# Performance work log

Measured on AMD Instinct MI355X. Metric: run time of the kernel, lower is better.

## Reference

```python
import jax, jax.numpy as jnp
import numpy as np

SIZE = 32  # CDIM internal attention resolution
DN = ('NCHW', 'OIHW', 'NCHW')


def conv3(x, w):
    # 3x3 (or matching SAME-size) conv, stride 1, padding SAME, no bias
    return jax.lax.conv_general_dilated(x, w, (1, 1), 'SAME', dimension_numbers=DN)


def bconv(x, w, s, b):
    # BBasicConv2d with BatchNorm folded (eval mode) into per-channel scale s and bias b, then ReLU
    return jax.nn.relu(conv3(x, w) * s[None, :, None, None] + b[None, :, None, None])


def spa_att(x, w):
    # SpatialAttention: sigmoid(conv([mean_c, max_c])) * x + x
    avg = jnp.mean(x, axis=1, keepdims=True)
    mx = jnp.max(x, axis=1, keepdims=True)
    a = conv3(jnp.concatenate([avg, mx], axis=1), w)
    return jax.nn.sigmoid(a) * x + x


def resize_bicubic(x, h, w):
    return jax.image.resize(x, (x.shape[0], x.shape[1], h, w), method='cubic')


def setup_inputs() -> dict:
    key = jax.random.key(0)
    ks = iter(jax.random.split(key, 64))
    B, C, H, W = 16, 64, 128, 128
    d = {}
    d['x'] = jax.random.normal(next(ks), (B, C, H, W), jnp.float32)
    d['y'] = jax.random.normal(next(ks), (B, C, H, W), jnp.float32)
    def qkv_params(pfx, cin):
        d[pfx + '_w'] = jax.random.normal(next(ks), (C, cin, 3, 3), jnp.float32) * 0.05
        d[pfx + '_s'] = jax.random.uniform(next(ks), (C,), jnp.float32, 0.5, 1.5)
        d[pfx + '_b'] = jax.random.normal(next(ks), (C,), jnp.float32) * 0.05
    for pfx in ['rq', 'rk', 'rv', 'iq', 'ik', 'iv']:
        qkv_params(pfx, C)
    d['red_w'] = jax.random.normal(next(ks), (C, 4 * C, 3, 3), jnp.float32) * 0.03
    d['red_s'] = jax.random.uniform(next(ks), (C,), jnp.float32, 0.5, 1.5)
    d['red_b'] = jax.random.normal(next(ks), (C,), jnp.float32) * 0.05
    d['sec_w'] = jax.random.normal(next(ks), (C, 3 * C, 3, 3), jnp.float32) * 0.03
    d['sec_s'] = jax.random.uniform(next(ks), (C,), jnp.float32, 0.5, 1.5)
    d['sec_b'] = jax.random.normal(next(ks), (C,), jnp.float32) * 0.05
    for g in ['g1', 'g2', 'g3', 'g4']:
        d[g] = jax.random.normal(next(ks), (1,), jnp.float32) * 0.1
    d['sa_r_w'] = jax.random.normal(next(ks), (1, 2, 3, 3), jnp.float32) * 0.1
    d['sa_i_w'] = jax.random.normal(next(ks), (1, 2, 3, 3), jnp.float32) * 0.1
    return d


def reference(x, y,
              rq_w, rq_s, rq_b, rk_w, rk_s, rk_b, rv_w, rv_s, rv_b,
              iq_w, iq_s, iq_b, ik_w, ik_s, ik_b, iv_w, iv_s, iv_b,
              red_w, red_s, red_b, sec_w, sec_s, sec_b,
              g1, g2, g3, g4, sa_r_w, sa_i_w):
    B, C, H, W = x.shape
    S = SIZE
    x_re = resize_bicubic(x, S, S)
    y_re = resize_bicubic(y, S, S)

    def qkv(z, qw, qs, qb, kw, ks_, kb, vw, vs, vb):
        Q = bconv(z, qw, qs, qb).reshape(B, -1, S * S)   # [B,C,S2]
        K = bconv(z, kw, ks_, kb).reshape(B, -1, S * S)  # [B,C,S2] (torch permutes later)
        V = bconv(z, vw, vs, vb).reshape(B, -1, S * S)
        return Q, K, V

    RQ, RK, RV = qkv(x_re, rq_w, rq_s, rq_b, rk_w, rk_s, rk_b, rv_w, rv_s, rv_b)
    IQ, IK, IV = qkv(y_re, iq_w, iq_s, iq_b, ik_w, ik_s, ik_b, iv_w, iv_s, iv_b)
    DV = RV + IV

    def attn(Q, K, V, orig, g):
        # mask = softmax(K^T @ Q, axis=-1): [B,S2,S2]
        mask = jax.nn.softmax(jnp.einsum('bcs,bct->bst', K, Q), axis=-1)
        # refine = V @ mask^T -> [B,C,S2]
        refine = jnp.einsum('bct,bst->bcs', V, mask).reshape(B, -1, S, S)
        refine = g.reshape(()) * refine
        return resize_bicubic(refine, orig.shape[2], orig.shape[3]) + orig

    RGB_refine = attn(RQ, RK, DV, x, g1)
    INF_refine = attn(IQ, IK, DV, y, g2)
    RGB_INF_refine = attn(RQ, IK, RV, y, g3)
    INF_RGB_refine = attn(IQ, RK, IV, x, g4)

    GLOBAL_ATT = bconv(jnp.concatenate([RGB_refine, INF_refine, RGB_INF_refine, INF_RGB_refine], axis=1),
                       red_w, red_s, red_b)
    rgb_spa = spa_att(x, sa_r_w)
    inf_spa = spa_att(y, sa_i_w)
    out = bconv(jnp.concatenate([GLOBAL_ATT, inf_spa, rgb_spa], axis=1), sec_w, sec_s, sec_b)
    return out
```

## Files before the change

kernel.cpp:

```cpp
#include <hip/hip_runtime.h>
#include <hip/hip_bf16.h>

#define B 16
#define C 64
#define H 128
#define W 128
#define S 32
#define S2 1024
#define HW 16384

typedef __attribute__((ext_vector_type(8))) short bf16x8;
typedef __attribute__((ext_vector_type(4))) float f32x4;
typedef __attribute__((ext_vector_type(8))) unsigned short u16x8;
typedef __attribute__((ext_vector_type(4))) unsigned short u16x4;

static __device__ __forceinline__ unsigned short f2bf(float v) {
    __hip_bfloat16 h = __float2bfloat16(v);
    return *reinterpret_cast<unsigned short*>(&h);
}
static __device__ __forceinline__ float bf2f(unsigned short u) {
    union { unsigned int i; float f; } cv;
    cv.i = ((unsigned int)u) << 16;
    return cv.f;
}

__device__ __forceinline__ float keys(float t) {
    t = fabsf(t);
    if (t >= 2.f) return 0.f;
    float t2 = t * t, t3 = t2 * t;
    if (t >= 1.f) return -0.5f * t3 + 2.5f * t2 - 4.f * t + 2.f;
    return 1.5f * t3 - 2.5f * t2 + 1.f;
}

__global__ void k_init(float* __restrict__ wd, float* __restrict__ wu) {
    int tid = threadIdx.x;
    if (tid < 32) {
        int i = tid;
        float sf = 4.f * i + 1.5f;
        int j0 = 4 * i - 6;
        float w[16];
        float s = 0.f;
        for (int k = 0; k < 16; k++) {
            int j = j0 + k;
            float v = 0.f;
            if (j >= 0 && j < 128) v = keys((sf - (float)j) * 0.25f);
            w[k] = v; s += v;
        }
        float inv = 1.f / s;
        for (int k = 0; k < 16; k++) wd[i * 16 + k] = w[k] * inv;
    } else if (tid >= 64 && tid < 192) {
        int i = tid - 64;
        float sf = 0.25f * i - 0.375f;
        int j0 = (int)floorf(sf) - 1;
        float w[4];
        float s = 0.f;
        for (int k = 0; k < 4; k++) {
            int j = j0 + k;
            float v = 0.f;
            if (j >= 0 && j < 32) v = keys(sf - (float)j);
            w[k] = v; s += v;
        }
        float inv = 1.f / s;
        for (int k = 0; k < 4; k++) wu[i * 4 + k] = w[k] * inv;
    }
}

__global__ void __launch_bounds__(256) k_down(const float* __restrict__ x, const float* __restrict__ y,
                                              const float* __restrict__ wd, unsigned short* __restrict__ re) {
    int bid = blockIdx.x;
    int img = bid >> 10;
    int bc = bid & 1023;
    const float* src = (img ? y : x) + (size_t)bc * HW;
    __shared__ unsigned short xsrc[128 * 128];
    __shared__ float tmp[32 * 160];
    __shared__ float wsh[512];
    int tid = threadIdx.x;
    for (int i = tid; i < 512; i += 256) wsh[i] = wd[i];
    #pragma unroll
    for (int it = 0; it < 16; ++it) {
        int i4 = (tid + it * 256) * 4;
        float4 v = *reinterpret_cast<const float4*>(src + i4);
        u16x4 o = {f2bf(v.x), f2bf(v.y), f2bf(v.z), f2bf(v.w)};
        *reinterpret_cast<u16x4*>(&xsrc[i4]) = o;
    }
    __syncthreads();
    #pragma unroll
    for (int it = 0; it < 16; ++it) {
        int idx = tid + it * 256;
        int oy = idx >> 7, xx = idx & 127;
        int j0 = 4 * oy - 6;
        float acc = 0.f;
        #pragma unroll
        for (int k = 0; k < 16; k++) {
            int j = j0 + k;
            if (j >= 0 && j < 128) acc += wsh[oy * 16 + k] * bf2f(xsrc[j * 128 + xx]);
        }
        tmp[oy * 160 + (xx & 3) * 40 + (xx >> 2)] = acc;
    }
    __syncthreads();
    #pragma unroll
    for (int it = 0; it < 4; ++it) {
        int idx = tid + it * 256;
        int oy = idx >> 5, ox = idx & 31;
        int j0 = 4 * ox - 6;
        float acc = 0.f;
        #pragma unroll
        for (int k = 0; k < 16; k++) {
            int j = j0 + k;
            if (j >= 0 && j < 128) acc += wsh[ox * 16 + k] * tmp[oy * 160 + (j & 3) * 40 + (j >> 2)];
        }
        re[(size_t)bid * 1024 + idx] = f2bf(acc);
    }
}

__global__ void k_wpack(const float* __restrict__ w, const float* __restrict__ s,
                        unsigned short* __restrict__ wpk, int cin) {
    int ks = blockIdx.x;
    int tid = threadIdx.x;
    int lane = tid & 63, ct = tid >> 6;
    int cb = ks / 9, kk = ks % 9;
    int m = ct * 16 + (lane & 15);
    int qq = lane >> 4;
    float sc = s[m];
    u16x8 outv;
    #pragma unroll
    for (int j = 0; j < 8; ++j) {
        int k = qq * 4 + (j & 3) + ((j >> 2) << 4);
        int ci = cb * 32 + k;
        float v = w[((size_t)m * cin + ci) * 9 + kk] * sc;
        outv[j] = f2bf(v);
    }
    *reinterpret_cast<u16x8*>(wpk + ((size_t)(ks * 4 + ct) * 64 + lane) * 8) = outv;
}

__global__ void k_wpackc(const float* __restrict__ w, const float* __restrict__ s,
                         unsigned short* __restrict__ wpk, int cin) {
    int ks = blockIdx.x;
    int tid = threadIdx.x;
    int lane = tid & 63, ct = tid >> 6;
    int cb = ks / 9, kk = ks % 9;
    int m = ct * 16 + (lane & 15);
    int qq = (lane >> 4) & 3;
    float sc = s[m];
    u16x8 outv;
    #pragma unroll
    for (int j = 0; j < 8; ++j) {
        int ci = cb * 32 + qq * 8 + j;
        float v = w[((size_t)m * cin + ci) * 9 + kk] * sc;
        outv[j] = f2bf(v);
    }
    *reinterpret_cast<u16x8*>(wpk + ((size_t)(ks * 4 + ct) * 64 + lane) * 8) = outv;
}

struct QkvBias { const float* b[6]; };

__global__ void __launch_bounds__(256) k_qkv2(const unsigned short* __restrict__ re,
                                              const unsigned short* __restrict__ wpkq,
                                              QkvBias bias,
                                              unsigned short* __restrict__ qt,
                                              unsigned short* __restrict__ kt,
                                              unsigned short* __restrict__ vn) {
    int bid = blockIdx.x;
    int q = bid >> 6;
    int rem = bid & 63;
    int b = rem >> 2;
    int quad = rem & 3;
    int img = (q < 3) ? 0 : 1;
    const unsigned short* src = re + ((size_t)(img * 16 + b)) * 64 * 1024;
    const bf16x8* wp = reinterpret_cast<const bf16x8*>(wpkq + (size_t)q * 18 * 4 * 64 * 8);
    const float* bptr = bias.b[q];

    int tid = threadIdx.x;
    int lane = tid & 63, w = tid >> 6;
    int l15 = lane & 15, qg = lane >> 4;

    __shared__ __align__(16) unsigned short xs[10 * 34 * 32];

    if (tid < 160) {
        int r = tid >> 4;
        int inner = tid & 15;
        int col = (inner >> 3) ? 33 : 0;
        int qd = inner & 7;
        int sbase = ((qd & 3) << 3) + ((qd >> 2) << 2);
        int sbs = sbase ^ ((((col >> 1) & 3)) << 3);
        u16x4 z = {0, 0, 0, 0};
        *reinterpret_cast<u16x4*>(&xs[(r * 34 + col) * 32 + sbs]) = z;
    }

    f32x4 acc[4][4] = {};

    for (int cb = 0; cb < 2; ++cb) {
        __syncthreads();
        #pragma unroll
        for (int tt = 0; tt < 2; ++tt) {
            int task = tid + tt * 256;
            if (task < 320) {
                int r = task >> 5;
                int inner = task & 31;
                int qd = inner >> 2, xc = inner & 3;
                int yy = quad * 8 - 1 + r;
                int x0 = xc * 8;
                int ci0 = cb * 32 + qd * 4;
                u16x8 v0, v1, v2, v3;
                if (yy >= 0 && yy < 32) {
                    const unsigned short* sp = src + (size_t)ci0 * 1024 + yy * 32 + x0;
                    v0 = *reinterpret_cast<const u16x8*>(sp);
                    v1 = *reinterpret_cast<const u16x8*>(sp + 1024);
                    v2 = *reinterpret_cast<const u16x8*>(sp + 2048);
                    v3 = *reinterpret_cast<const u16x8*>(sp + 3072);
                } else {
                    v0 = (u16x8)0; v1 = (u16x8)0; v2 = (u16x8)0; v3 = (u16x8)0;
                }
                int sbase = ((qd & 3) << 3) + ((qd >> 2) << 2);
                #pragma unroll
                for (int dx = 0; dx < 8; ++dx) {
                    int col = x0 + 1 + dx;
                    int sbs = sbase ^ (((col >> 1) & 3) << 3);
                    u16x4 pk = {v0[dx], v1[dx], v2[dx], v3[dx]};
                    *reinterpret_cast<u16x4*>(&xs[(r * 34 + col) * 32 + sbs]) = pk;
                }
            }
        }
        __syncthreads();
        #pragma unroll
        for (int ky = 0; ky < 3; ++ky) {
            #pragma unroll
            for (int kx = 0; kx < 3; ++kx) {
                int ksidx = cb * 9 + ky * 3 + kx;
                bf16x8 afr[4];
                #pragma unroll
                for (int ct = 0; ct < 4; ++ct)
                    afr[ct] = wp[((size_t)(ksidx * 4 + ct) << 6) + lane];
                bf16x8 bfr[4];
                #pragma unroll
                for (int nt = 0; nt < 4; ++nt) {
                    int rp = nt >> 1;
                    int col = (nt & 1) * 16 + l15 + kx;
                    int r = w * 2 + rp + ky;
                    int sbs = (qg ^ ((col >> 1) & 3)) << 3;
                    bfr[nt] = *reinterpret_cast<const bf16x8*>(&xs[(r * 34 + col) * 32 + sbs]);
                }
                #pragma unroll
                for (int ct = 0; ct < 4; ++ct)
                    #pragma unroll
                    for (int nt = 0; nt < 4; ++nt)
                        acc[ct][nt] = __builtin_amdgcn_mfma_f32_16x16x32_bf16(afr[ct], bfr[nt], acc[ct][nt], 0, 0, 0);
            }
        }
    }

    int pair = (q < 3) ? 0 : 1;
    bool isV = (q == 2 || q == 5);
    unsigned short* dst;
    if (q == 0 || q == 3)      dst = qt + ((size_t)(pair * 16 + b)) * 65536;
    else if (q == 1 || q == 4) dst = kt + ((size_t)(pair * 16 + b)) * 65536;
    else                       dst = vn + ((size_t)(pair * 16 + b)) * 65536;
    #pragma unroll
    for (int ct = 0; ct < 4; ++ct) {
        float4 bi = *reinterpret_cast<const float4*>(bptr + ct * 16 + qg * 4);
        #pragma unroll
        for (int nt = 0; nt < 4; ++nt) {
            int pxl = nt * 16 + l15;
            int rowg = quad * 8 + w * 2 + (pxl >> 5);
            int colg = pxl & 31;
            int px = rowg * 32 + colg;
            #pragma unroll
            for (int reg = 0; reg < 4; ++reg) {
                int co = ct * 16 + qg * 4 + reg;
                float bv = (reg == 0) ? bi.x : (reg == 1) ? bi.y : (reg == 2) ? bi.z : bi.w;
                float v = fmaxf(acc[ct][nt][reg] + bv, 0.f);
                unsigned short bf = f2bf(v);
                if (isV) dst[(size_t)co * 1024 + px] = bf;
                else     dst[(size_t)px * 64 + co] = bf;
            }
        }
    }
}

__global__ void k_packa(const unsigned short* __restrict__ qt,
                        const unsigned short* __restrict__ kt,
                        unsigned short* __restrict__ qtf,
                        unsigned short* __restrict__ ktf) {
    int bid = blockIdx.x;
    int tsel = bid >> 7;
    int b = (bid >> 3) & 15;
    int seg = bid & 7;
    int tid = threadIdx.x;
    int lane = tid & 63, w = tid >> 6;
    int l15 = lane & 15, qg = lane >> 4;
    const unsigned short* src = (tsel < 2 ? qt : kt) + ((size_t)((tsel & 1) * 16 + b)) * 65536;
    unsigned short* dst = (tsel < 2 ? qtf : ktf) + ((size_t)((tsel & 1) * 16 + b)) * 65536;
    #pragma unroll
    for (int it = 0; it < 4; ++it) {
        int fi = seg * 16 + it * 4 + w;
        int tf = fi >> 1, kb = fi & 1;
        const unsigned short* row = src + (size_t)(tf * 16 + l15) * 64 + kb * 32 + qg * 4;
        u16x4 a0 = *reinterpret_cast<const u16x4*>(row);
        u16x4 a1 = *reinterpret_cast<const u16x4*>(row + 16);
        u16x8 o;
        #pragma unroll
        for (int j = 0; j < 4; ++j) { o[j] = a0[j]; o[4 + j] = a1[j]; }
        *reinterpret_cast<u16x8*>(dst + (size_t)fi * 512 + lane * 8) = o;
    }
}

__global__ void k_packv(const unsigned short* __restrict__ vn,
                        unsigned short* __restrict__ vf) {
    int bid = blockIdx.x;
    int b = bid >> 3;
    int seg = bid & 7;
    int tid = threadIdx.x;
    int lane = tid & 63, w = tid >> 6;
    int l15 = lane & 15, qg = lane >> 4;
    const unsigned short* rv = vn + (size_t)b * 65536;
    const unsigned short* iv = vn + (size_t)(16 + b) * 65536;
    #pragma unroll
    for (int it = 0; it < 4; ++it) {
        int fi = seg * 16 + it * 4 + w;
        int cf = fi >> 5, tq = fi & 31;
        int c = cf * 16 + l15;
        size_t roff = (size_t)c * 1024 + tq * 32 + qg * 4;
        u16x4 r0 = *reinterpret_cast<const u16x4*>(rv + roff);
        u16x4 r1 = *reinterpret_cast<const u16x4*>(rv + roff + 16);
        u16x4 i0 = *reinterpret_cast<const u16x4*>(iv + roff);
        u16x4 i1 = *reinterpret_cast<const u16x4*>(iv + roff + 16);
        u16x8 orv, oiv, odv;
        #pragma unroll
        for (int j = 0; j < 4; ++j) {
            orv[j] = r0[j]; orv[4 + j] = r1[j];
            oiv[j] = i0[j]; oiv[4 + j] = i1[j];
            odv[j] = f2bf(bf2f(r0[j]) + bf2f(i0[j]));
            odv[4 + j] = f2bf(bf2f(r1[j]) + bf2f(i1[j]));
        }
        size_t eoff = ((size_t)b * 128 + fi) * 512 + lane * 8;
        *reinterpret_cast<u16x8*>(vf + eoff) = orv;
        *reinterpret_cast<u16x8*>(vf + 1048576 + eoff) = oiv;
        *reinterpret_cast<u16x8*>(vf + 2097152 + eoff) = odv;
    }
}

__global__ void __launch_bounds__(256) k_attn3(const unsigned short* __restrict__ QTF,
                                               const unsigned short* __restrict__ KTF,
                                               const unsigned short* __restrict__ VF,
                                               float* __restrict__ ref) {
    int bid = blockIdx.x;
    int a = bid >> 10;
    int b = (bid >> 6) & 15;
    int stile = bid & 63;
    int qsel = (a == 0 || a == 2) ? 0 : 1;
    int ksel = (a == 0 || a == 3) ? 0 : 1;
    int vsel = (a < 2) ? 2 : (a == 2 ? 0 : 1);

    int tid = threadIdx.x;
    int lane = tid & 63, w = tid >> 6;
    int l15 = lane & 15, qg = lane >> 4;

    const bf16x8* qf = reinterpret_cast<const bf16x8*>(QTF) + ((size_t)(qsel * 16 + b) * 128) * 64;
    const bf16x8* kf = reinterpret_cast<const bf16x8*>(KTF) + ((size_t)(ksel * 16 + b) * 128) * 64;
    const bf16x8* vfb = reinterpret_cast<const bf16x8*>(VF) + ((size_t)(vsel * 16 + b) * 128) * 64;

    __shared__ float mxw[4][16];
    __shared__ float smw[4][16];
    __shared__ float rbuf[4][64 * 16];

    bf16x8 bk0 = kf[(size_t)(stile * 2 + 0) * 64 + lane];
    bf16x8 bk1 = kf[(size_t)(stile * 2 + 1) * 64 + lane];
    f32x4 acc[16] = {};
    #pragma unroll
    for (int mf = 0; mf < 16; ++mf) {
        int tf = w * 16 + mf;
        bf16x8 a0 = qf[(size_t)(tf * 2 + 0) * 64 + lane];
        bf16x8 a1 = qf[(size_t)(tf * 2 + 1) * 64 + lane];
        acc[mf] = __builtin_amdgcn_mfma_f32_16x16x32_bf16(a0, bk0, acc[mf], 0, 0, 0);
        acc[mf] = __builtin_amdgcn_mfma_f32_16x16x32_bf16(a1, bk1, acc[mf], 0, 0, 0);
    }

    float mx = -1e30f;
    #pragma unroll
    for (int mf = 0; mf < 16; ++mf)
        #pragma unroll
        for (int r = 0; r < 4; ++r) mx = fmaxf(mx, acc[mf][r]);
    mx = fmaxf(mx, __shfl_xor(mx, 16));
    mx = fmaxf(mx, __shfl_xor(mx, 32));
    if (qg == 0) mxw[w][l15] = mx;
    __syncthreads();
    float M = fmaxf(fmaxf(mxw[0][l15], mxw[1][l15]), fmaxf(mxw[2][l15], mxw[3][l15]));
    float sm = 0.f;
    #pragma unroll
    for (int mf = 0; mf < 16; ++mf)
        #pragma unroll
        for (int r = 0; r < 4; ++r) {
            float e = __builtin_amdgcn_exp2f((acc[mf][r] - M) * 1.4426950408889634f);
            acc[mf][r] = e;
            sm += e;
        }
    sm += __shfl_xor(sm, 16);
    sm += __shfl_xor(sm, 32);
    if (qg == 0) smw[w][l15] = sm;
    __syncthreads();
    float inv = 1.f / (smw[0][l15] + smw[1][l15] + smw[2][l15] + smw[3][l15]);

    f32x4 pacc[4] = {};
    #pragma unroll
    for (int kk = 0; kk < 8; ++kk) {
        bf16x8 bp;
        #pragma unroll
        for (int j = 0; j < 4; ++j) {
            bp[j] = (short)f2bf(acc[2 * kk][j]);
            bp[4 + j] = (short)f2bf(acc[2 * kk + 1][j]);
        }
        #pragma unroll
        for (int cf = 0; cf < 4; ++cf) {
            bf16x8 av = vfb[(size_t)(cf * 32 + w * 8 + kk) * 64 + lane];
            pacc[cf] = __builtin_amdgcn_mfma_f32_16x16x32_bf16(av, bp, pacc[cf], 0, 0, 0);
        }
    }
    #pragma unroll
    for (int cf = 0; cf < 4; ++cf)
        #pragma unroll
        for (int r = 0; r < 4; ++r)
            rbuf[w][(cf * 16 + qg * 4 + r) * 16 + l15] = pacc[cf][r] * inv;
    __syncthreads();

    {
        int c = tid >> 2, sg = tid & 3;
        f32x4 o;
        #pragma unroll
        for (int k2 = 0; k2 < 4; ++k2) {
            int idx = c * 16 + sg * 4 + k2;
            o[k2] = rbuf[0][idx] + rbuf[1][idx] + rbuf[2][idx] + rbuf[3][idx];
        }
        *reinterpret_cast<f32x4*>(ref + (((size_t)a * 16 + b) * 64 + c) * 1024 + stile * 16 + sg * 4) = o;
    }
}

__global__ void __launch_bounds__(256) k_up3(const float* __restrict__ ref, const float* __restrict__ wu,
                                             const float* __restrict__ x, const float* __restrict__ y,
                                             const float* __restrict__ g1, const float* __restrict__ g2,
                                             const float* __restrict__ g3, const float* __restrict__ g4,
                                             __hip_bfloat16* __restrict__ cat4) {
    int bid = blockIdx.x;
    int b = bid >> 7;
    int c = (bid >> 1) & 63;
    int pair = bid & 1;
    int aA = pair ? 1 : 0;
    int aB = pair ? 2 : 3;
    const float* orig = (pair ? y : x) + ((size_t)b * 64 + c) * HW;
    float gA = (pair ? g2 : g1)[0];
    float gB = (pair ? g3 : g4)[0];
    const float* srcA = ref + (((size_t)aA * 16 + b) * 64 + c) * 1024;
    const float* srcB = ref + (((size_t)aB * 16 + b) * 64 + c) * 1024;

    __shared__ float wsh[512];
    __shared__ float rch[2][1024];
    __shared__ float tmp[2][128][32];
    int tid = threadIdx.x;
    for (int i = tid; i < 512; i += 256) wsh[i] = wu[i];
    {
        float4 a4 = reinterpret_cast<const float4*>(srcA)[tid];
        float4 b4 = reinterpret_cast<const float4*>(srcB)[tid];
        reinterpret_cast<float4*>(&rch[0][0])[tid] = a4;
        reinterpret_cast<float4*>(&rch[1][0])[tid] = b4;
    }
    __syncthreads();

    #pragma unroll
    for (int it = 0; it < 4; ++it) {
        int task = tid + it * 256;
        int u = task >> 5, xx = task & 31;
        float w0[5], w1[5];
        #pragma unroll
        for (int m = 0; m < 5; ++m) {
            int j = u - 2 + m;
            bool ok = (j >= 0) && (j < 32);
            w0[m] = ok ? rch[0][j * 32 + xx] : 0.f;
            w1[m] = ok ? rch[1][j * 32 + xx] : 0.f;
        }
        #pragma unroll
        for (int r = 0; r < 4; ++r) {
            int oy = 4 * u + r;
            int mo = r >> 1;
            float a0 = 0.f, a1 = 0.f;
            #pragma unroll
            for (int k = 0; k < 4; ++k) {
                float wv = wsh[oy * 4 + k];
                a0 += wv * w0[mo + k];
                a1 += wv * w1[mo + k];
            }
            tmp[0][oy][xx] = a0;
            tmp[1][oy][xx] = a1;
        }
    }
    __syncthreads();

    size_t obA = ((size_t)b * 256 + aA * 64 + c) * HW;
    size_t obB = ((size_t)b * 256 + aB * 64 + c) * HW;
    unsigned short* cat = (unsigned short*)cat4;
    #pragma unroll
    for (int it = 0; it < 16; ++it) {
        int task = tid + it * 256;
        int oy = task >> 5, t = task & 31;
        float u0[5], u1[5];
        #pragma unroll
        for (int m = 0; m < 5; ++m) {
            int j = t - 2 + m;
            bool ok = (j >= 0) && (j < 32);
            u0[m] = ok ? tmp[0][oy][j] : 0.f;
            u1[m] = ok ? tmp[1][oy][j] : 0.f;
        }
        float4 ov = *reinterpret_cast<const float4*>(orig + oy * 128 + t * 4);
        float ovr[4] = {ov.x, ov.y, ov.z, ov.w};
        u16x4 oA, oB;
        #pragma unroll
        for (int r = 0; r < 4; ++r) {
            int ox = 4 * t + r;
            int mo = r >> 1;
            float a0 = 0.f, a1 = 0.f;
            #pragma unroll
            for (int k = 0; k < 4; ++k) {
                float wv = wsh[ox * 4 + k];
                a0 += wv * u0[mo + k];
                a1 += wv * u1[mo + k];
            }
            oA[r] = f2bf(gA * a0 + ovr[r]);
            oB[r] = f2bf(gB * a1 + ovr[r]);
        }
        *reinterpret_cast<u16x4*>(&cat[obA + oy * 128 + t * 4]) = oA;
        *reinterpret_cast<u16x4*>(&cat[obB + oy * 128 + t * 4]) = oB;
    }
}

__global__ void k_mm(const float* __restrict__ x, const float* __restrict__ y,
                     float* __restrict__ mm) {
    int bid = blockIdx.x;
    int img = bid >> 7;
    int rem = bid & 127;
    int b = rem >> 3;
    int chunk = rem & 7;
    const float* src = (img ? y : x) + (size_t)b * 64 * HW;
    int tid = threadIdx.x;
    size_t base = ((size_t)(img * 16 + b)) * 2 * HW;
    for (int i = 0; i < 8; i++) {
        int px = chunk * 2048 + i * 256 + tid;
        float s = 0.f, mx = -1e30f;
        for (int c = 0; c < 64; c++) {
            float v = src[(size_t)c * HW + px];
            s += v;
            mx = fmaxf(mx, v);
        }
        mm[base + px] = s * (1.f / 64.f);
        mm[base + HW + px] = mx;
    }
}

__global__ void k_spaconv(const float* __restrict__ mm, const float* __restrict__ saw_r,
                          const float* __restrict__ saw_i, float* __restrict__ sig) {
    int bid = blockIdx.x;
    int img = bid >> 7;
    int rem = bid & 127;
    int b = rem >> 3;
    int chunk = rem & 7;
    const float* w = img ? saw_i : saw_r;
    __shared__ float wsh[18];
    if (threadIdx.x < 18) wsh[threadIdx.x] = w[threadIdx.x];
    __syncthreads();
    const float* m0 = mm + ((size_t)(img * 16 + b)) * 2 * HW;
    for (int i = 0; i < 8; i++) {
        int px = chunk * 2048 + i * 256 + threadIdx.x;
        int yy = px >> 7, xx = px & 127;
        float acc = 0.f;
        #pragma unroll
        for (int ch = 0; ch < 2; ch++) {
            const float* m = m0 + (size_t)ch * HW;
            #pragma unroll
            for (int dy = 0; dy < 3; dy++)
                #pragma unroll
                for (int dx = 0; dx < 3; dx++) {
                    int iy = yy + dy - 1, ix = xx + dx - 1;
                    if (iy >= 0 && iy < 128 && ix >= 0 && ix < 128)
                        acc += wsh[ch * 9 + dy * 3 + dx] * m[iy * 128 + ix];
                }
        }
        sig[((size_t)(img * 16 + b)) * HW + px] = 1.f / (1.f + expf(-acc));
    }
}

__global__ void k_scale(const float* __restrict__ x, const float* __restrict__ y,
                        const float* __restrict__ sig, unsigned short* __restrict__ sxy) {
    int gid = blockIdx.x * 256 + threadIdx.x;
    int part = gid >> 21;
    int b = (gid >> 17) & 15;
    int c = (gid >> 11) & 63;
    int t8 = gid & 2047;
    int px = t8 * 8;
    const float* src = (part ? x : y) + ((size_t)b * 64 + c) * HW + px;
    const float* sg = sig + ((size_t)((part ? 0 : 16) + b)) * HW + px;
    u16x8 o;
    #pragma unroll
    for (int j = 0; j < 8; ++j) o[j] = f2bf(src[j] * (1.f + sg[j]));
    *reinterpret_cast<u16x8*>(sxy + ((size_t)b * 128 + part * 64 + c) * HW + px) = o;
}

template<int CIBLKS, bool OBF16>
__global__ void __launch_bounds__(512, 1) k_conv(const unsigned short* __restrict__ srcA, int cinA,
                                                 const unsigned short* __restrict__ srcB,
                                                 const unsigned short* __restrict__ wpk,
                                                 const float* __restrict__ bias,
                                                 void* __restrict__ outp) {
    const int cinB = CIBLKS * 32 - cinA;
    int bid = blockIdx.x;
    int b = bid >> 5, rt = bid & 31;
    int y0 = rt * 4;
    int tid = threadIdx.x;
    int lane = tid & 63, w = tid >> 6;
    int l15 = lane & 15, qg = (lane >> 4) & 3;
    int wr = w >> 1, wc = w & 1;

    __shared__ __align__(16) unsigned short xs[6 * 133 * 32];
    __shared__ __align__(16) unsigned short ws2[9 * 4 * 64 * 8];

    if (tid < 48) {
        int r = tid >> 3;
        int rem = tid & 7;
        int col = (rem >> 2) ? 129 : 0;
        int q = rem & 3;
        int slot = q ^ ((col >> 2) & 3);
        u16x8 z = (u16x8)0;
        *reinterpret_cast<u16x8*>(&xs[(r * 133 + col) * 32 + slot * 8]) = z;
    }

    f32x4 acc[4][4] = {};
    const bf16x8* wp = reinterpret_cast<const bf16x8*>(wpk);

    for (int cb = 0; cb < CIBLKS; ++cb) {
        __syncthreads();
        {
            const bf16x8* wsrc = wp + (size_t)cb * 2304;
            bf16x8* wdst = reinterpret_cast<bf16x8*>(ws2);
            #pragma unroll
            for (int e = 0; e < 4; ++e)
                wdst[tid + e * 512] = wsrc[tid + e * 512];
            if (tid < 256) wdst[tid + 2048] = wsrc[tid + 2048];
        }
        #pragma unroll
        for (int tt = 0; tt < 2; ++tt) {
            int task = tid + tt * 512;
            if (task < 768) {
                int q8 = task / 192;
                int rr = (task % 192) >> 5;
                int xq = task & 31;
                int yy = y0 - 1 + rr;
                int x0 = xq * 4;
                int ci0 = cb * 32 + q8 * 8;
                u16x4 v[8];
                if (yy >= 0 && yy < 128) {
                    const unsigned short* sp;
                    if (ci0 < cinA) sp = srcA + ((size_t)b * cinA + ci0) * HW;
                    else            sp = srcB + ((size_t)b * cinB + (ci0 - cinA)) * HW;
                    sp += yy * 128 + x0;
                    #pragma unroll
                    for (int p = 0; p < 8; ++p)
                        v[p] = *reinterpret_cast<const u16x4*>(sp + p * HW);
                } else {
                    #pragma unroll
                    for (int p = 0; p < 8; ++p) v[p] = (u16x4)0;
                }
                #pragma unroll
                for (int i = 0; i < 4; ++i) {
                    int d = (i + xq) & 3;
                    int col = x0 + 1 + d;
                    int slot = q8 ^ ((col >> 2) & 3);
                    u16x8 o;
                    #pragma unroll
                    for (int p = 0; p < 8; ++p) o[p] = v[p][d];
                    *reinterpret_cast<u16x8*>(&xs[(rr * 133 + col) * 32 + slot * 8]) = o;
                }
            }
        }
        __syncthreads();
        __builtin_amdgcn_s_setprio(1);
        #pragma unroll
        for (int ky = 0; ky < 3; ++ky) {
            #pragma unroll
            for (int kx = 0; kx < 3; ++kx) {
                int kk = ky * 3 + kx;
                bf16x8 afr[4];
                #pragma unroll
                for (int ct = 0; ct < 4; ++ct)
                    afr[ct] = *reinterpret_cast<const bf16x8*>(&ws2[((kk * 4 + ct) * 64 + lane) * 8]);
                int row = wr + ky;
                bf16x8 bfr[4];
                #pragma unroll
                for (int nt = 0; nt < 4; ++nt) {
                    int col = wc * 64 + nt * 16 + l15 + kx;
                    int slot = qg ^ ((col >> 2) & 3);
                    bfr[nt] = *reinterpret_cast<const bf16x8*>(&xs[(row * 133 + col) * 32 + slot * 8]);
                }
                #pragma unroll
                for (int ct = 0; ct < 4; ++ct)
                    #pragma unroll
                    for (int nt = 0; nt < 4; ++nt)
                        acc[ct][nt] = __builtin_amdgcn_mfma_f32_16x16x32_bf16(afr[ct], bfr[nt], acc[ct][nt], 0, 0, 0);
            }
        }
        __builtin_amdgcn_s_setprio(0);
    }

    int row_out = y0 + wr;
    #pragma unroll
    for (int ct = 0; ct < 4; ++ct) {
        float4 bi = *reinterpret_cast<const float4*>(bias + ct * 16 + qg * 4);
        #pragma unroll
        for (int nt = 0; nt < 4; ++nt) {
            int col_out = wc * 64 + nt * 16 + l15;
            #pragma unroll
            for (int reg = 0; reg < 4; ++reg) {
                int co = ct * 16 + qg * 4 + reg;
                float bv = (reg == 0) ? bi.x : (reg == 1) ? bi.y : (reg == 2) ? bi.z : bi.w;
                float v = fmaxf(acc[ct][nt][reg] + bv, 0.f);
                size_t off = ((size_t)b * 64 + co) * HW + row_out * 128 + col_out;
                if (OBF16) ((unsigned short*)outp)[off] = f2bf(v);
                else       ((float*)outp)[off] = v;
            }
        }
    }
}

extern "C" void kernel_launch(void* const* d_in, const int* in_sizes, int n_in,
                              void* d_out, int out_size, void* d_ws, size_t ws_size,
                              hipStream_t stream) {
    const float* x = (const float*)d_in[0];
    const float* y = (const float*)d_in[1];

    const float* qw[6]; const float* qs[6];
    QkvBias qb;
    for (int q = 0; q < 6; q++) {
        qw[q] = (const float*)d_in[2 + 3 * q];
        qs[q] = (const float*)d_in[3 + 3 * q];
        qb.b[q] = (const float*)d_in[4 + 3 * q];
    }
    const float* red_w = (const float*)d_in[20];
    const float* red_s = (const float*)d_in[21];
    const float* red_b = (const float*)d_in[22];
    const float* sec_w = (const float*)d_in[23];
    const float* sec_s = (const float*)d_in[24];
    const float* sec_b = (const float*)d_in[25];
    const float* g1 = (const float*)d_in[26];
    const float* g2 = (const float*)d_in[27];
    const float* g3 = (const float*)d_in[28];
    const float* g4 = (const float*)d_in[29];
    const float* sa_r_w = (const float*)d_in[30];
    const float* sa_i_w = (const float*)d_in[31];

    float* WD = (float*)d_ws;
    float* WU = WD + 512;
    float* SIG = WU + 512;
    float* MM = SIG + 524288;
    float* REF = MM + 1048576;
    unsigned short* WPKR = (unsigned short*)(REF + 4194304);
    unsigned short* WPKS = WPKR + 147456;
    unsigned short* WPKQ = WPKS + 110592;
    unsigned short* REB = WPKQ + 221184;
    unsigned short* QT  = REB + 2097152;
    unsigned short* KT  = QT + 2097152;
    unsigned short* VN  = KT + 2097152;
    unsigned short* GATT = VN + 2097152;
    unsigned short* CAT4 = GATT + 16777216;
    unsigned short* QTF = CAT4;
    unsigned short* KTF = CAT4 + 2097152;
    unsigned short* VF  = CAT4 + 4194304;
    unsigned short* SECXY = CAT4;

    k_init<<<1, 256, 0, stream>>>(WD, WU);
    k_down<<<2 * 16 * 64, 256, 0, stream>>>(x, y, WD, REB);
    for (int q = 0; q < 6; q++)
        k_wpack<<<18, 256, 0, stream>>>(qw[q], qs[q], WPKQ + (size_t)q * 36864, 64);
    k_wpackc<<<72, 256, 0, stream>>>(red_w, red_s, WPKR, 256);
    k_wpackc<<<54, 256, 0, stream>>>(sec_w, sec_s, WPKS, 192);
    k_qkv2<<<6 * 64, 256, 0, stream>>>(REB, WPKQ, qb, QT, KT, VN);
    k_packa<<<512, 256, 0, stream>>>(QT, KT, QTF, KTF);
    k_packv<<<128, 256, 0, stream>>>(VN, VF);
    k_attn3<<<4 * 16 * 64, 256, 0, stream>>>(QTF, KTF, VF, REF);
    k_up3<<<16 * 128, 256, 0, stream>>>(REF, WU, x, y, g1, g2, g3, g4, (__hip_bfloat16*)CAT4);
    k_mm<<<2 * 16 * 8, 256, 0, stream>>>(x, y, MM);
    k_spaconv<<<2 * 16 * 8, 256, 0, stream>>>(MM, sa_r_w, sa_i_w, SIG);
    k_conv<8, true><<<16 * 32, 512, 0, stream>>>(CAT4, 256, CAT4, WPKR, red_b, GATT);
    k_scale<<<16384, 256, 0, stream>>>(x, y, SIG, SECXY);
    k_conv<6, false><<<16 * 32, 512, 0, stream>>>(GATT, 64, SECXY, WPKS, sec_b, d_out);
}
```

Before: 556.3 us.

## Halve conv weight LDS buffer to fit two blocks per CU, change swizzle

```diff
diff --git a/kernel.cpp b/kernel.cpp
--- a/kernel.cpp
+++ b/kernel.cpp
@@ -602,7 +602,7 @@
 }
 
 template<int CIBLKS, bool OBF16>
-__global__ void __launch_bounds__(512, 1) k_conv(const unsigned short* __restrict__ srcA, int cinA,
+__global__ void __launch_bounds__(512, 2) k_conv(const unsigned short* __restrict__ srcA, int cinA,
                                                  const unsigned short* __restrict__ srcB,
                                                  const unsigned short* __restrict__ wpk,
                                                  const float* __restrict__ bias,
@@ -617,30 +617,29 @@
     int wr = w >> 1, wc = w & 1;
 
     __shared__ __align__(16) unsigned short xs[6 * 133 * 32];
-    __shared__ __align__(16) unsigned short ws2[9 * 4 * 64 * 8];
+    __shared__ __align__(16) unsigned short ws2[5 * 4 * 64 * 8];
 
     if (tid < 48) {
         int r = tid >> 3;
         int rem = tid & 7;
         int col = (rem >> 2) ? 129 : 0;
         int q = rem & 3;
-        int slot = q ^ ((col >> 2) & 3);
+        int slot = q ^ (((col >> 2) ^ (col >> 4)) & 3);
         u16x8 z = (u16x8)0;
         *reinterpret_cast<u16x8*>(&xs[(r * 133 + col) * 32 + slot * 8]) = z;
     }
 
     f32x4 acc[4][4] = {};
     const bf16x8* wp = reinterpret_cast<const bf16x8*>(wpk);
+    bf16x8* wdst = reinterpret_cast<bf16x8*>(ws2);
 
     for (int cb = 0; cb < CIBLKS; ++cb) {
         __syncthreads();
         {
             const bf16x8* wsrc = wp + (size_t)cb * 2304;
-            bf16x8* wdst = reinterpret_cast<bf16x8*>(ws2);
-            #pragma unroll
-            for (int e = 0; e < 4; ++e)
-                wdst[tid + e * 512] = wsrc[tid + e * 512];
-            if (tid < 256) wdst[tid + 2048] = wsrc[tid + 2048];
+            wdst[tid] = wsrc[tid];
+            wdst[tid + 512] = wsrc[tid + 512];
+            if (tid < 256) wdst[tid + 1024] = wsrc[tid + 1024];
         }
         #pragma unroll
         for (int tt = 0; tt < 2; ++tt) {
@@ -669,7 +668,7 @@
                 for (int i = 0; i < 4; ++i) {
                     int d = (i + xq) & 3;
                     int col = x0 + 1 + d;
-                    int slot = q8 ^ ((col >> 2) & 3);
+                    int slot = q8 ^ (((col >> 2) ^ (col >> 4)) & 3);
                     u16x8 o;
                     #pragma unroll
                     for (int p = 0; p < 8; ++p) o[p] = v[p][d];
@@ -680,28 +679,55 @@
         __syncthreads();
         __builtin_amdgcn_s_setprio(1);
         #pragma unroll
-        for (int ky = 0; ky < 3; ++ky) {
-            #pragma unroll
-            for (int kx = 0; kx < 3; ++kx) {
-                int kk = ky * 3 + kx;
-                bf16x8 afr[4];
+        for (int kk = 0; kk < 5; ++kk) {
+            int ky = kk / 3, kx = kk % 3;
+            bf16x8 afr[4];
+            #pragma unroll
+            for (int ct = 0; ct < 4; ++ct)
+                afr[ct] = *reinterpret_cast<const bf16x8*>(&ws2[((kk * 4 + ct) * 64 + lane) * 8]);
+            int row = wr + ky;
+            bf16x8 bfr[4];
+            #pragma unroll
+            for (int nt = 0; nt < 4; ++nt) {
+                int col = wc * 64 + nt * 16 + l15 + kx;
+                int slot = qg ^ (((col >> 2) ^ (col >> 4)) & 3);
+                bfr[nt] = *reinterpret_cast<const bf16x8*>(&xs[(row * 133 + col) * 32 + slot * 8]);
+            }
+            #pragma unroll
+            for (int ct = 0; ct < 4; ++ct)
                 #pragma unroll
-                for (int ct = 0; ct < 4; ++ct)
-                    afr[ct] = *reinterpret_cast<const bf16x8*>(&ws2[((kk * 4 + ct) * 64 + lane) * 8]);
-                int row = wr + ky;
-                bf16x8 bfr[4];
+                for (int nt = 0; nt < 4; ++nt)
+                    acc[ct][nt] = __builtin_amdgcn_mfma_f32_16x16x32_bf16(afr[ct], bfr[nt], acc[ct][nt], 0, 0, 0);
+        }
+        __builtin_amdgcn_s_setprio(0);
+        __syncthreads();
+        {
+            const bf16x8* wsrc = wp + (size_t)cb * 2304 + 1280;
+            wdst[tid] = wsrc[tid];
+            wdst[tid + 512] = wsrc[tid + 512];
+        }
+        __syncthreads();
+        __builtin_amdgcn_s_setprio(1);
+        #pragma unroll
+        for (int kk = 5; kk < 9; ++kk) {
+            int ky = kk / 3, kx = kk % 3;
+            bf16x8 afr[4];
+            #pragma unroll
+            for (int ct = 0; ct < 4; ++ct)
+                afr[ct] = *reinterpret_cast<const bf16x8*>(&ws2[(((kk - 5) * 4 + ct) * 64 + lane) * 8]);
+            int row = wr + ky;
+            bf16x8 bfr[4];
+            #pragma unroll
+            for (int nt = 0; nt < 4; ++nt) {
+                int col = wc * 64 + nt * 16 + l15 + kx;
+                int slot = qg ^ (((col >> 2) ^ (col >> 4)) & 3);
+                bfr[nt] = *reinterpret_cast<const bf16x8*>(&xs[(row * 133 + col) * 32 + slot * 8]);
+            }
+            #pragma unroll
+            for (int ct = 0; ct < 4; ++ct)
                 #pragma unroll
-                for (int nt = 0; nt < 4; ++nt) {
-                    int col = wc * 64 + nt * 16 + l15 + kx;
-                    int slot = qg ^ ((col >> 2) & 3);
-                    bfr[nt] = *reinterpret_cast<const bf16x8*>(&xs[(row * 133 + col) * 32 + slot * 8]);
-                }
-                #pragma unroll
-                for (int ct = 0; ct < 4; ++ct)
-                    #pragma unroll
-                    for (int nt = 0; nt < 4; ++nt)
-                        acc[ct][nt] = __builtin_amdgcn_mfma_f32_16x16x32_bf16(afr[ct], bfr[nt], acc[ct][nt], 0, 0, 0);
-            }
+                for (int nt = 0; nt < 4; ++nt)
+                    acc[ct][nt] = __builtin_amdgcn_mfma_f32_16x16x32_bf16(afr[ct], bfr[nt], acc[ct][nt], 0, 0, 0);
         }
         __builtin_amdgcn_s_setprio(0);
     }
```

After: 573.4 us. 1.03x slower.

## Fuse channel mean/max, spatial-attention conv and scaling into one kernel

Applied to the files above, without the earlier changes.

```diff
diff --git a/kernel.cpp b/kernel.cpp
--- a/kernel.cpp
+++ b/kernel.cpp
@@ -530,75 +530,89 @@
     }
 }
 
-__global__ void k_mm(const float* __restrict__ x, const float* __restrict__ y,
-                     float* __restrict__ mm) {
+__global__ void __launch_bounds__(256) k_spa(const float* __restrict__ x, const float* __restrict__ y,
+                                             const float* __restrict__ saw_r, const float* __restrict__ saw_i,
+                                             unsigned short* __restrict__ sxy) {
     int bid = blockIdx.x;
     int img = bid >> 7;
     int rem = bid & 127;
     int b = rem >> 3;
     int chunk = rem & 7;
     const float* src = (img ? y : x) + (size_t)b * 64 * HW;
-    int tid = threadIdx.x;
-    size_t base = ((size_t)(img * 16 + b)) * 2 * HW;
-    for (int i = 0; i < 8; i++) {
-        int px = chunk * 2048 + i * 256 + tid;
-        float s = 0.f, mx = -1e30f;
-        for (int c = 0; c < 64; c++) {
-            float v = src[(size_t)c * HW + px];
-            s += v;
-            mx = fmaxf(mx, v);
-        }
-        mm[base + px] = s * (1.f / 64.f);
-        mm[base + HW + px] = mx;
-    }
-}
-
-__global__ void k_spaconv(const float* __restrict__ mm, const float* __restrict__ saw_r,
-                          const float* __restrict__ saw_i, float* __restrict__ sig) {
-    int bid = blockIdx.x;
-    int img = bid >> 7;
-    int rem = bid & 127;
-    int b = rem >> 3;
-    int chunk = rem & 7;
     const float* w = img ? saw_i : saw_r;
+    int part = img ? 0 : 1;
+    int gy0 = chunk * 16;
+
+    __shared__ float avgsh[18 * 128];
+    __shared__ float maxsh[18 * 128];
+    __shared__ float sigsh[16 * 128];
     __shared__ float wsh[18];
-    if (threadIdx.x < 18) wsh[threadIdx.x] = w[threadIdx.x];
+    int tid = threadIdx.x;
+    if (tid < 18) wsh[tid] = w[tid];
+
+    #pragma unroll
+    for (int it = 0; it < 3; ++it) {
+        int task = tid + it * 256;
+        if (task < 576) {
+            int r = task >> 5;
+            int q4 = task & 31;
+            int gy = gy0 - 1 + r;
+            float sx = 0.f, sy = 0.f, sz = 0.f, sw = 0.f;
+            float mxx = 0.f, mxy = 0.f, mxz = 0.f, mxw2 = 0.f;
+            if (gy >= 0 && gy < 128) {
+                mxx = mxy = mxz = mxw2 = -1e30f;
+                const float* p = src + gy * 128 + q4 * 4;
+                for (int c = 0; c < 64; ++c) {
+                    float4 v = *reinterpret_cast<const float4*>(p + (size_t)c * HW);
+                    sx += v.x; sy += v.y; sz += v.z; sw += v.w;
+                    mxx = fmaxf(mxx, v.x); mxy = fmaxf(mxy, v.y);
+                    mxz = fmaxf(mxz, v.z); mxw2 = fmaxf(mxw2, v.w);
+                }
+                sx *= (1.f / 64.f); sy *= (1.f / 64.f); sz *= (1.f / 64.f); sw *= (1.f / 64.f);
+            }
+            int o = r * 128 + q4 * 4;
+            avgsh[o + 0] = sx; avgsh[o + 1] = sy; avgsh[o + 2] = sz; avgsh[o + 3] = sw;
+            maxsh[o + 0] = mxx; maxsh[o + 1] = mxy; maxsh[o + 2] = mxz; maxsh[o + 3] = mxw2;
+        }
+    }
     __syncthreads();
-    const float* m0 = mm + ((size_t)(img * 16 + b)) * 2 * HW;
-    for (int i = 0; i < 8; i++) {
-        int px = chunk * 2048 + i * 256 + threadIdx.x;
-        int yy = px >> 7, xx = px & 127;
+
+    #pragma unroll
+    for (int it = 0; it < 8; ++it) {
+        int px = tid + it * 256;
+        int ly = px >> 7, xx = px & 127;
         float acc = 0.f;
         #pragma unroll
-        for (int ch = 0; ch < 2; ch++) {
-            const float* m = m0 + (size_t)ch * HW;
+        for (int dy = 0; dy < 3; ++dy) {
+            int r = ly + dy;
             #pragma unroll
-            for (int dy = 0; dy < 3; dy++)
-                #pragma unroll
-                for (int dx = 0; dx < 3; dx++) {
-                    int iy = yy + dy - 1, ix = xx + dx - 1;
-                    if (iy >= 0 && iy < 128 && ix >= 0 && ix < 128)
-                        acc += wsh[ch * 9 + dy * 3 + dx] * m[iy * 128 + ix];
+            for (int dx = 0; dx < 3; ++dx) {
+                int ix = xx + dx - 1;
+                if (ix >= 0 && ix < 128) {
+                    acc += wsh[dy * 3 + dx] * avgsh[r * 128 + ix];
+                    acc += wsh[9 + dy * 3 + dx] * maxsh[r * 128 + ix];
                 }
-        }
-        sig[((size_t)(img * 16 + b)) * HW + px] = 1.f / (1.f + expf(-acc));
-    }
-}
-
-__global__ void k_scale(const float* __restrict__ x, const float* __restrict__ y,
-                        const float* __restrict__ sig, unsigned short* __restrict__ sxy) {
-    int gid = blockIdx.x * 256 + threadIdx.x;
-    int part = gid >> 21;
-    int b = (gid >> 17) & 15;
-    int c = (gid >> 11) & 63;
-    int t8 = gid & 2047;
-    int px = t8 * 8;
-    const float* src = (part ? x : y) + ((size_t)b * 64 + c) * HW + px;
-    const float* sg = sig + ((size_t)((part ? 0 : 16) + b)) * HW + px;
-    u16x8 o;
-    #pragma unroll
-    for (int j = 0; j < 8; ++j) o[j] = f2bf(src[j] * (1.f + sg[j]));
-    *reinterpret_cast<u16x8*>(sxy + ((size_t)b * 128 + part * 64 + c) * HW + px) = o;
+            }
+        }
+        sigsh[px] = 1.f / (1.f + expf(-acc));
+    }
+    __syncthreads();
+
+    float sg[8];
+    #pragma unroll
+    for (int k = 0; k < 8; ++k) sg[k] = 1.f + sigsh[tid * 8 + k];
+    unsigned short* dst = sxy + ((size_t)b * 128 + part * 64) * HW + gy0 * 128;
+    const float* sb = src + gy0 * 128;
+    for (int c = 0; c < 64; ++c) {
+        #pragma unroll
+        for (int j = 0; j < 2; ++j) {
+            int px = tid * 8 + j * 4;
+            float4 v = *reinterpret_cast<const float4*>(sb + (size_t)c * HW + px);
+            u16x4 o = {f2bf(v.x * sg[j * 4 + 0]), f2bf(v.y * sg[j * 4 + 1]),
+                       f2bf(v.z * sg[j * 4 + 2]), f2bf(v.w * sg[j * 4 + 3])};
+            *reinterpret_cast<u16x4*>(dst + (size_t)c * HW + px) = o;
+        }
+    }
 }
 
 template<int CIBLKS, bool OBF16>
@@ -782,9 +796,7 @@
     k_packv<<<128, 256, 0, stream>>>(VN, VF);
     k_attn3<<<4 * 16 * 64, 256, 0, stream>>>(QTF, KTF, VF, REF);
     k_up3<<<16 * 128, 256, 0, stream>>>(REF, WU, x, y, g1, g2, g3, g4, (__hip_bfloat16*)CAT4);
-    k_mm<<<2 * 16 * 8, 256, 0, stream>>>(x, y, MM);
-    k_spaconv<<<2 * 16 * 8, 256, 0, stream>>>(MM, sa_r_w, sa_i_w, SIG);
     k_conv<8, true><<<16 * 32, 512, 0, stream>>>(CAT4, 256, CAT4, WPKR, red_b, GATT);
-    k_scale<<<16384, 256, 0, stream>>>(x, y, SIG, SECXY);
+    k_spa<<<2 * 16 * 8, 256, 0, stream>>>(x, y, sa_r_w, sa_i_w, SECXY);
     k_conv<6, false><<<16 * 32, 512, 0, stream>>>(GATT, 64, SECXY, WPKS, sec_b, d_out);
 }
```

After: 523.5 us, median of 2. 1.06x faster.
